# Kernel optimization log

Hardware: AMD Instinct MI355X
Metric: run time of the kernel (lower is better)

The kernel has to match this reference:

```python
import jax, jax.numpy as jnp
import numpy as np
import math

EPS = 1e-6
P_MIN = 1e-3
P_MAX = 10.0
NUM_ITERS = 3
REG = 1.0
K = 64       # num_clusters
D = 128      # cluster_dim
TOKEN = 256  # token_dim
B, N, C = 8, 8192, 512


def _l2norm(t):
    return t / jnp.clip(jnp.linalg.norm(t, axis=-1, keepdims=True), 1e-12)


def _mlp(h, W1, b1, W2, b2):
    # torch Linear: y = h @ W.T + b ; dropout is identity at eval
    return jax.nn.relu(h @ W1.T + b1) @ W2.T + b2


def _log_otp_solver(log_a, log_b, M, num_iters, reg):
    M = M / reg
    u = jnp.zeros_like(log_a)
    v = jnp.zeros_like(log_b)
    for _ in range(num_iters):  # fixed small iteration count
        u = log_a - jax.scipy.special.logsumexp(M + v[:, None, :], axis=2)
        v = log_b - jax.scipy.special.logsumexp(M + u[:, :, None], axis=1)
    return M + u[:, :, None] + v[:, None, :]


def _get_matching_probs(S, dustbin_score, num_iters, reg):
    b, m, n = S.shape
    dust_row = jnp.broadcast_to(dustbin_score, (b, 1, n)).astype(S.dtype)
    S_aug = jnp.concatenate([S, dust_row], axis=1)  # [b, m+1, n]
    norm = -math.log(n + m)
    log_a = jnp.full((m + 1,), norm, dtype=S.dtype).at[-1].add(math.log(n - m))
    log_a = jnp.broadcast_to(log_a, (b, m + 1))
    log_b = jnp.full((b, n), norm, dtype=S.dtype)
    log_P = _log_otp_solver(log_a, log_b, S_aug, num_iters, reg)
    return log_P - norm


def setup_inputs() -> dict:
    key = jax.random.key(0)
    ks = jax.random.split(key, 8)
    x = jax.random.normal(ks[0], (B, N, C), dtype=jnp.float32)

    def lin(k, fin, fout):
        k1, k2 = jax.random.split(k)
        W = 0.02 * jax.random.normal(k1, (fout, fin), dtype=jnp.float32)
        b = 0.02 * jax.random.normal(k2, (fout,), dtype=jnp.float32)
        return W, b

    tW1, tb1 = lin(ks[1], C, 512)
    tW2, tb2 = lin(ks[2], 512, TOKEN)
    cW1, cb1 = lin(ks[3], C, 512)
    cW2, cb2 = lin(ks[4], 512, D)
    sW1, sb1 = lin(ks[5], C, 512)
    sW2, sb2 = lin(ks[6], 512, K)
    # GeM p param init so that softplus(w)+p_min == 3.0
    gem_w = jnp.array([math.log(math.exp(3.0 - P_MIN) - 1.0)], dtype=jnp.float32)
    dust_bin = jnp.array(1.0, dtype=jnp.float32)
    return dict(x=x, gem_w=gem_w, dust_bin=dust_bin,
                tW1=tW1, tb1=tb1, tW2=tW2, tb2=tb2,
                cW1=cW1, cb1=cb1, cW2=cW2, cb2=cb2,
                sW1=sW1, sb1=sb1, sW2=sW2, sb2=sb2)


def reference(x, gem_w, dust_bin,
              tW1, tb1, tW2, tb2,
              cW1, cb1, cW2, cb2,
              sW1, sb1, sW2, sb2):
    # --- GeM pooling: [B, N, C] -> [B, C] ---
    p = jnp.minimum(jax.nn.softplus(gem_w) + P_MIN, P_MAX)  # [1]
    g = jnp.mean(jnp.clip(x.astype(jnp.float32), EPS, None) ** p, axis=1) ** (1.0 / p)
    g = jnp.where(jnp.isfinite(g), g, jnp.zeros_like(g))

    global_token = _mlp(g, tW1, tb1, tW2, tb2)          # [B, TOKEN]
    local = _mlp(x, cW1, cb1, cW2, cb2)                 # [B, N, D]
    scores = _mlp(x, sW1, sb1, sW2, sb2)                # [B, N, K]

    S = scores.transpose(0, 2, 1)                       # [B, K, N]
    log_P = _get_matching_probs(S, dust_bin, NUM_ITERS, REG)  # [B, K+1, N]
    p_mat = jnp.exp(log_P)[:, :-1, :]                   # drop dustbin -> [B, K, N]

    # aggregated[b, d, k] = sum_n local[b, n, d] * p[b, k, n]  (no O(B*D*K*N) blowup)
    agg = jnp.einsum('bnd,bkn->bdk', local, p_mat).reshape(x.shape[0], -1)  # [B, D*K]

    result = jnp.concatenate([_l2norm(global_token), _l2norm(agg)], axis=-1)
    return _l2norm(result)
```

## Files before the change

kernel.cpp:

```cpp
#include <hip/hip_runtime.h>
#include <hip/hip_bf16.h>
#include <math.h>

#define BB   8
#define NN   8192
#define CC   512
#define DD   128
#define KK   64
#define TOK  256
#define MM   (BB*NN)

typedef unsigned short u16;
typedef __attribute__((ext_vector_type(8))) short short8;
typedef __attribute__((ext_vector_type(4))) float floatx4;

struct PtrSz { const void* p[15]; int sz[15]; };

__device__ __forceinline__ float bf2f(u16 v) {
    union { unsigned u; float f; } x; x.u = ((unsigned)v) << 16; return x.f;
}
__device__ __forceinline__ u16 f2bf(float f) {
    union { float f; unsigned u; } x; x.f = f;
    unsigned r = x.u + 0x7fffu + ((x.u >> 16) & 1u);
    return (u16)(r >> 16);
}
__device__ __forceinline__ float nat_exp2(float a) {
    float r; asm("v_exp_f32 %0, %1" : "=v"(r) : "v"(a)); return r;
}
__device__ __forceinline__ float nat_log2(float a) {
    float r; asm("v_log_f32 %0, %1" : "=v"(r) : "v"(a)); return r;
}
__device__ __forceinline__ void gload16(const void* g, void* l) {
    __builtin_amdgcn_global_load_lds(
        (const __attribute__((address_space(1))) void*)g,
        (__attribute__((address_space(3))) void*)l, 16, 0, 0);
}

__global__ __launch_bounds__(256)
void fill_sentinel(float* __restrict__ out, int n, float val) {
    int i = blockIdx.x*256 + threadIdx.x;
    if (i < n) out[i] = val;
}

__global__ __launch_bounds__(256)
void detect_all(PtrSz ps, int* __restrict__ flags) {
    int i = blockIdx.x;
    const u16* q = (const u16*)ps.p[i];
    int m = ps.sz[i] < 4096 ? ps.sz[i] : 4096;
    __shared__ int cnt;
    if (threadIdx.x == 0) cnt = 0;
    __syncthreads();
    int c = 0;
    for (int j = threadIdx.x; j < m; j += 256) {
        int e = (q[j] >> 7) & 0xFF;
        if (e < 90 || e > 165) c++;
    }
    atomicAdd(&cnt, c);
    __syncthreads();
    if (threadIdx.x == 0) flags[i] = (cnt * 8 > m) ? 1 : 0;
}

#define W_TW1 0
#define W_TB1 262144
#define W_TW2 262656
#define W_TB2 393728
#define W_CW1 393984
#define W_CB1 656128
#define W_CW2 656640
#define W_CB2 722176
#define W_SW1 722304
#define W_SB1 984448
#define W_SW2 984960
#define W_SB2 1017728
#define W_TOTAL 1017792

__global__ __launch_bounds__(256)
void conv_weights(PtrSz ps, const int* __restrict__ flags,
                  u16* __restrict__ wbuf, float* __restrict__ wscal) {
    long gid = (long)blockIdx.x*256 + threadIdx.x;
    if (gid == 0) {
        float vb = bf2f(((const u16*)ps.p[1])[0]);
        float vf = ((const float*)ps.p[1])[0];
        wscal[0] = (fabsf(vb - 2.94694f) < 0.2f) ? vb : vf;
    } else if (gid == 1) {
        float vb = bf2f(((const u16*)ps.p[2])[0]);
        float vf = ((const float*)ps.p[2])[0];
        wscal[1] = (fabsf(vb - 1.0f) < 0.2f) ? vb : vf;
    }
    if (gid >= W_TOTAL) return;
    int idx; long off;
    if      (gid < W_TB1) { idx = 3;  off = W_TW1; }
    else if (gid < W_TW2) { idx = 4;  off = W_TB1; }
    else if (gid < W_TB2) { idx = 5;  off = W_TW2; }
    else if (gid < W_CW1) { idx = 6;  off = W_TB2; }
    else if (gid < W_CB1) { idx = 7;  off = W_CW1; }
    else if (gid < W_CW2) { idx = 8;  off = W_CB1; }
    else if (gid < W_CB2) { idx = 9;  off = W_CW2; }
    else if (gid < W_SW1) { idx = 10; off = W_CB2; }
    else if (gid < W_SB1) { idx = 11; off = W_SW1; }
    else if (gid < W_SW2) { idx = 12; off = W_SB1; }
    else if (gid < W_SB2) { idx = 13; off = W_SW2; }
    else                  { idx = 14; off = W_SB2; }
    long k = gid - off;
    bool f32in = flags[idx] != 0;
    wbuf[gid] = f32in ? f2bf(((const float*)ps.p[idx])[k]) : ((const u16*)ps.p[idx])[k];
}

__global__ __launch_bounds__(256)
void gem_partial(const void* __restrict__ x, const float* __restrict__ wscal,
                 const int* __restrict__ flags, float* __restrict__ gacc) {
    __shared__ float red[4][512];
    int b = blockIdx.x, ny = blockIdx.y;
    int tid  = threadIdx.x;
    int wave = tid >> 6, lane = tid & 63;
    bool f32in = (flags[0] != 0);
    float gw = wscal[0];
    float p  = fminf(log1pf(expf(gw)) + 1e-3f, 10.0f);
    int c0 = lane*8;
    float s[8];
#pragma unroll
    for (int j = 0; j < 8; ++j) s[j] = 0.f;
    size_t base = ((size_t)b*NN + (size_t)ny*64 + wave)*CC + c0;
    if (f32in) {
        const float* xf = (const float*)x;
#pragma unroll 4
        for (int n = 0; n < 64; n += 4) {
            const float* pf = xf + base + (size_t)n*CC;
            float4 x0 = *(const float4*)pf;
            float4 x1 = *(const float4*)(pf + 4);
            float xv[8] = {x0.x,x0.y,x0.z,x0.w,x1.x,x1.y,x1.z,x1.w};
#pragma unroll
            for (int j = 0; j < 8; ++j)
                s[j] += nat_exp2(p * nat_log2(fmaxf(xv[j], 1e-6f)));
        }
    } else {
        const u16* xu = (const u16*)x;
#pragma unroll 4
        for (int n = 0; n < 64; n += 4) {
            short8 v8 = *(const short8*)(xu + base + (size_t)n*CC);
#pragma unroll
            for (int j = 0; j < 8; ++j)
                s[j] += nat_exp2(p * nat_log2(fmaxf(bf2f((u16)v8[j]), 1e-6f)));
        }
    }
#pragma unroll
    for (int j = 0; j < 8; ++j) red[wave][c0 + j] = s[j];
    __syncthreads();
#pragma unroll
    for (int t = 0; t < 2; ++t) {
        int c = tid + t*256;
        float v = red[0][c] + red[1][c] + red[2][c] + red[3][c];
        atomicAdd(&gacc[b*CC + c], v);
    }
}

__global__ __launch_bounds__(256)
void gem_finalize(const float* __restrict__ gacc, const float* __restrict__ wscal,
                  float* __restrict__ g) {
    int i = blockIdx.x*256 + threadIdx.x;
    float gw = wscal[0];
    float p  = fminf(log1pf(expf(gw)) + 1e-3f, 10.0f);
    float m  = gacc[i] / (float)NN;
    float r  = powf(m, 1.0f/p);
    if (!isfinite(r)) r = 0.f;
    g[i] = r;
}

__global__ __launch_bounds__(512)
void token_mlp(const float* __restrict__ g, const u16* __restrict__ wbuf,
               float* __restrict__ t) {
    __shared__ float gs[CC];
    __shared__ float hs[512];
    int b = blockIdx.x, j = threadIdx.x;
    gs[j] = g[b*CC + j];
    __syncthreads();
    float a = bf2f(wbuf[W_TB1 + j]);
    const u16* w = wbuf + W_TW1 + (size_t)j*CC;
    for (int c = 0; c < CC; ++c) a += gs[c]*bf2f(w[c]);
    hs[j] = fmaxf(a, 0.f);
    __syncthreads();
    if (j < TOK) {
        float a2 = bf2f(wbuf[W_TB2 + j]);
        const u16* w2 = wbuf + W_TW2 + (size_t)j*512;
        for (int c = 0; c < 512; ++c) a2 += hs[c]*bf2f(w2[c]);
        t[b*TOK + j] = a2;
    }
}

template<int BN, int MODE, bool RELU, bool ARAW>
__global__ __launch_bounds__(256)
void gemm_bt(const void* __restrict__ A, const u16* __restrict__ W,
             const u16* __restrict__ bias, void* __restrict__ Cout,
             const int* __restrict__ flags, int N, int Ksz,
             size_t a_base, int bidx_ovr) {
    constexpr int WSUB_N = BN/32;
    extern __shared__ char smem[];
    u16* a_lds = (u16*)smem;
    u16* b_lds = (u16*)smem + 128*32;
    const int tid  = threadIdx.x;
    const int wave = tid >> 6, lane = tid & 63;
    const int wm = wave >> 1, wn = wave & 1;

    int bx = blockIdx.x, by = blockIdx.y;
    {
        int nbx = gridDim.x, nby = gridDim.y;
        int nwg = nbx*nby;
        if ((nwg & 7) == 0) {
            int lid = bx + by*nbx;
            int q = nwg >> 3;
            int t = (lid & 7)*q + (lid >> 3);
            by = t % nby;
            bx = t / nby;
        }
    }
    const int bm0 = bx * 128;
    const int bn0 = by * BN;
    const int fr = lane & 15;
    const int fk = (lane >> 4) * 8;
    const bool f32in = ARAW && (flags[0] != 0);

    floatx4 acc[4][WSUB_N];
#pragma unroll
    for (int i = 0; i < 4; ++i)
#pragma unroll
        for (int j = 0; j < WSUB_N; ++j) acc[i][j] = (floatx4){0.f,0.f,0.f,0.f};

    for (int k0 = 0; k0 < Ksz; k0 += 32) {
        if (f32in) {
#pragma unroll
            for (int part = 0; part < 2; ++part) {
                int chunk = part*256 + tid;
                int row = chunk >> 2, kc = (chunk & 3)*8;
                size_t gidx = a_base + (size_t)(bm0 + row)*Ksz + k0 + kc;
                const float* pf = (const float*)A + gidx;
                float4 x0 = *(const float4*)pf;
                float4 x1 = *(const float4*)(pf + 4);
                short8 vA;
                vA[0]=(short)f2bf(x0.x); vA[1]=(short)f2bf(x0.y);
                vA[2]=(short)f2bf(x0.z); vA[3]=(short)f2bf(x0.w);
                vA[4]=(short)f2bf(x1.x); vA[5]=(short)f2bf(x1.y);
                vA[6]=(short)f2bf(x1.z); vA[7]=(short)f2bf(x1.w);
                *(short8*)(a_lds + row*32 + kc) = vA;
            }
        } else {
#pragma unroll
            for (int part = 0; part < 2; ++part) {
                int cb = part*256 + wave*64;
                int mych = cb + lane;
                int row = mych >> 2, kc = (mych & 3)*8;
                gload16((const u16*)A + a_base + (size_t)(bm0 + row)*Ksz + k0 + kc,
                        a_lds + (size_t)cb*8);
            }
        }
#pragma unroll
        for (int part = 0; part < BN/64; ++part) {
            int cb = part*256 + wave*64;
            int mych = cb + lane;
            int row = mych >> 2, kc = (mych & 3)*8;
            gload16(W + (size_t)(bn0 + row)*Ksz + k0 + kc,
                    b_lds + (size_t)cb*8);
        }
        __syncthreads();
        short8 af[4], bfr[WSUB_N];
#pragma unroll
        for (int i = 0; i < 4; ++i)
            af[i] = *(const short8*)(a_lds + (wm*64 + i*16 + fr)*32 + fk);
#pragma unroll
        for (int j = 0; j < WSUB_N; ++j)
            bfr[j] = *(const short8*)(b_lds + (wn*WSUB_N*16 + j*16 + fr)*32 + fk);
#pragma unroll
        for (int i = 0; i < 4; ++i)
#pragma unroll
            for (int j = 0; j < WSUB_N; ++j)
                acc[i][j] = __builtin_amdgcn_mfma_f32_16x16x32_bf16(af[i], bfr[j], acc[i][j], 0, 0, 0);
        __syncthreads();
    }

    if constexpr (MODE == 0) {
        u16* C = (u16*)Cout;
#pragma unroll
        for (int i = 0; i < 4; ++i) {
            int row0 = wm*64 + i*16 + ((lane>>4)<<2);
#pragma unroll
            for (int j = 0; j < WSUB_N; ++j) {
                int col = wn*WSUB_N*16 + j*16 + fr;
                float bb = bf2f(bias[bn0+col]);
#pragma unroll
                for (int r = 0; r < 4; ++r) {
                    float v = acc[i][j][r] + bb;
                    if (RELU) v = fmaxf(v, 0.f);
                    C[(size_t)(bm0+row0+r)*N + (bn0+col)] = f2bf(v);
                }
            }
        }
    } else {
        const int bidx = (bidx_ovr >= 0) ? bidx_ovr : (bm0 >> 13);
        const int nin  = bm0 & 8191;
        if constexpr (MODE == 1) {
            u16* tr = (u16*)smem;
#pragma unroll
            for (int i = 0; i < 4; ++i) {
                int row0 = wm*64 + i*16 + ((lane>>4)<<2);
#pragma unroll
                for (int j = 0; j < WSUB_N; ++j) {
                    int col = wn*WSUB_N*16 + j*16 + fr;
                    float bb = bf2f(bias[bn0+col]);
#pragma unroll
                    for (int r = 0; r < 4; ++r) {
                        float v = acc[i][j][r] + bb;
                        if (RELU) v = fmaxf(v, 0.f);
                        tr[col*128 + row0 + r] = f2bf(v);
                    }
                }
            }
            __syncthreads();
            u16* O = (u16*)Cout;
#pragma unroll
            for (int c = 0; c < (BN*128)/256; ++c) {
                int flat = c*256 + tid;
                int dcol = flat >> 7, rr = flat & 127;
                O[(size_t)(bidx*BN + bn0 + dcol)*NN + nin + rr] = tr[dcol*128 + rr];
            }
        } else {
            float* tr = (float*)smem;
#pragma unroll
            for (int i = 0; i < 4; ++i) {
                int row0 = wm*64 + i*16 + ((lane>>4)<<2);
#pragma unroll
                for (int j = 0; j < WSUB_N; ++j) {
                    int col = wn*WSUB_N*16 + j*16 + fr;
                    float bb = bf2f(bias[bn0+col]);
#pragma unroll
                    for (int r = 0; r < 4; ++r) {
                        float v = acc[i][j][r] + bb;
                        if (RELU) v = fmaxf(v, 0.f);
                        tr[col*128 + row0 + r] = v;
                    }
                }
            }
            __syncthreads();
            float* O = (float*)Cout;
#pragma unroll
            for (int c = 0; c < (BN*128)/256; ++c) {
                int flat = c*256 + tid;
                int dcol = flat >> 7, rr = flat & 127;
                O[(size_t)(bidx*BN + bn0 + dcol)*NN + nin + rr] = tr[dcol*128 + rr];
            }
        }
    }
}

__global__ __launch_bounds__(256)
void sink_u(const float* __restrict__ ST, const float* __restrict__ v,
            const float* __restrict__ wscal, float* __restrict__ u) {
    int m = blockIdx.x, b = blockIdx.y, t = threadIdx.x;
    const float norm = -logf(8256.0f);
    float la = (m == 64) ? norm + logf(8128.0f) : norm;
    float dustf = wscal[1];
    const float* vb = v + (size_t)b*NN;
    float r[32];
    float mx = -1e30f;
    if (m < 64) {
        const float* row = ST + ((size_t)b*64 + m)*NN;
#pragma unroll
        for (int i = 0; i < 32; ++i) { int n = t + i*256; r[i] = row[n] + vb[n]; mx = fmaxf(mx, r[i]); }
    } else {
#pragma unroll
        for (int i = 0; i < 32; ++i) { int n = t + i*256; r[i] = dustf + vb[n]; mx = fmaxf(mx, r[i]); }
    }
#pragma unroll
    for (int off = 32; off; off >>= 1) mx = fmaxf(mx, __shfl_xor(mx, off));
    __shared__ float red[4];
    if ((t & 63) == 0) red[t>>6] = mx;
    __syncthreads();
    mx = fmaxf(fmaxf(red[0], red[1]), fmaxf(red[2], red[3]));
    __syncthreads();
    float s = 0.f;
#pragma unroll
    for (int i = 0; i < 32; ++i) s += expf(r[i] - mx);
#pragma unroll
    for (int off = 32; off; off >>= 1) s += __shfl_xor(s, off);
    if ((t & 63) == 0) red[t>>6] = s;
    __syncthreads();
    s = red[0] + red[1] + red[2] + red[3];
    if (t == 0) u[b*65 + m] = la - (mx + logf(s));
}

__global__ __launch_bounds__(256)
void sink_v(const float* __restrict__ ST, const float* __restrict__ u,
            const float* __restrict__ wscal, float* __restrict__ v) {
    int b = blockIdx.y;
    int n = blockIdx.x*256 + threadIdx.x;
    __shared__ float us[65];
    if (threadIdx.x < 65) us[threadIdx.x] = u[b*65 + threadIdx.x];
    __syncthreads();
    const float norm = -logf(8256.0f);
    float mx = wscal[1] + us[64];
    float s  = 1.0f;
    const float* col = ST + (size_t)b*64*NN + n;
    for (int m = 0; m < 64; ++m) {
        float tv = col[(size_t)m*NN] + us[m];
        float nm = fmaxf(mx, tv);
        s = s*expf(mx - nm) + expf(tv - nm);
        mx = nm;
    }
    v[(size_t)b*NN + n] = norm - (mx + logf(s));
}

__global__ __launch_bounds__(256)
void sink_p(const float* __restrict__ ST, const float* __restrict__ u,
            const float* __restrict__ v, u16* __restrict__ P) {
    int b = blockIdx.y;
    int n = blockIdx.x*256 + threadIdx.x;
    const float norm = -logf(8256.0f);
    float vn = v[(size_t)b*NN + n];
    for (int k = 0; k < 64; ++k) {
        float lp = ST[((size_t)b*64 + k)*NN + n] + u[b*65 + k] + vn - norm;
        P[((size_t)b*64 + k)*NN + n] = f2bf(expf(lp));
    }
}

__global__ __launch_bounds__(256)
void agg_mfma(const u16* __restrict__ localT, const u16* __restrict__ P,
              float* __restrict__ agg) {
    __shared__ u16 a_lds[128*32];
    __shared__ u16 b_lds[64*32];
    int b = blockIdx.y, ns = blockIdx.x;
    int n0 = ns*256;
    const int tid  = threadIdx.x;
    const int wave = tid >> 6, lane = tid & 63;
    const int wm = wave >> 1, wn = wave & 1;
    const int fr = lane & 15, fk = (lane >> 4)*8;

    floatx4 acc[4][2];
#pragma unroll
    for (int i = 0; i < 4; ++i)
#pragma unroll
        for (int j = 0; j < 2; ++j) acc[i][j] = (floatx4){0.f,0.f,0.f,0.f};

    for (int s = 0; s < 8; ++s) {
        int nk = n0 + s*32;
#pragma unroll
        for (int part = 0; part < 2; ++part) {
            int chunk = part*256 + tid;
            int row = chunk >> 2, kc = (chunk & 3)*8;
            short8 vA = *(const short8*)(localT + ((size_t)b*128 + row)*NN + nk + kc);
            *(short8*)(a_lds + row*32 + kc) = vA;
        }
        {
            int row = tid >> 2, kc = (tid & 3)*8;
            short8 vB = *(const short8*)(P + ((size_t)b*64 + row)*NN + nk + kc);
            *(short8*)(b_lds + row*32 + kc) = vB;
        }
        __syncthreads();
        short8 af[4], bfr[2];
#pragma unroll
        for (int i = 0; i < 4; ++i)
            af[i] = *(const short8*)(a_lds + (wm*64 + i*16 + fr)*32 + fk);
#pragma unroll
        for (int j = 0; j < 2; ++j)
            bfr[j] = *(const short8*)(b_lds + (wn*32 + j*16 + fr)*32 + fk);
#pragma unroll
        for (int i = 0; i < 4; ++i)
#pragma unroll
            for (int j = 0; j < 2; ++j)
                acc[i][j] = __builtin_amdgcn_mfma_f32_16x16x32_bf16(af[i], bfr[j], acc[i][j], 0, 0, 0);
        __syncthreads();
    }
#pragma unroll
    for (int i = 0; i < 4; ++i) {
        int d0 = wm*64 + i*16 + ((lane>>4)<<2);
#pragma unroll
        for (int j = 0; j < 2; ++j) {
            int k = wn*32 + j*16 + fr;
#pragma unroll
            for (int r = 0; r < 4; ++r)
                atomicAdd(&agg[(size_t)b*8192 + (d0+r)*64 + k], acc[i][j][r]);
        }
    }
}

__global__ __launch_bounds__(256)
void finalize_out(const float* __restrict__ tg, const float* __restrict__ agg,
                  float* __restrict__ out) {
    int b = blockIdx.x, tid = threadIdx.x;
    float tv = tg[b*TOK + tid];
    float s1 = tv*tv;
    const float* ab = agg + (size_t)b*8192;
    float av[32];
    float s2 = 0.f;
#pragma unroll
    for (int i = 0; i < 32; ++i) { av[i] = ab[tid + i*256]; s2 += av[i]*av[i]; }
#pragma unroll
    for (int off = 32; off; off >>= 1) { s1 += __shfl_xor(s1, off); s2 += __shfl_xor(s2, off); }
    __shared__ float r1[4], r2[4];
    int wave = tid >> 6, lane = tid & 63;
    if (lane == 0) { r1[wave] = s1; r2[wave] = s2; }
    __syncthreads();
    float S1 = r1[0]+r1[1]+r1[2]+r1[3];
    float S2 = r2[0]+r2[1]+r2[2]+r2[3];
    const float rs2 = 1.41421356237f;
    float sc1 = 1.0f/(fmaxf(sqrtf(S1), 1e-12f)*rs2);
    float sc2 = 1.0f/(fmaxf(sqrtf(S2), 1e-12f)*rs2);
    out[(size_t)b*8448 + tid] = tv*sc1;
#pragma unroll
    for (int i = 0; i < 32; ++i)
        out[(size_t)b*8448 + 256 + tid + i*256] = av[i]*sc2;
}

extern "C" void kernel_launch(void* const* d_in, const int* in_sizes, int n_in,
                              void* d_out, int out_size, void* d_ws, size_t ws_size,
                              hipStream_t stream) {
    float* out = (float*)d_out;

    static const int EXP[15] = {33554432,1,1,262144,512,131072,256,
                                262144,512,65536,128,262144,512,32768,64};
    bool ok = (n_in == 15) && (out_size == 67584);
    if (ok) for (int i = 0; i < 15; ++i) ok = ok && (in_sizes[i] == EXP[i]);
    if (!ok) {
        fill_sentinel<<<264, 256, 0, stream>>>(out, out_size, 0.25f);
        return;
    }
    const size_t NEED_BATCH = 52934656ull;
    if (ws_size < NEED_BATCH) {
        fill_sentinel<<<264, 256, 0, stream>>>(out, out_size, 0.5f);
        return;
    }

    const void* x = d_in[0];
    PtrSz ps;
    for (int i = 0; i < 15; ++i) { ps.p[i] = d_in[i]; ps.sz[i] = in_sizes[i]; }

    char* base = (char*)d_ws;
    float* gacc = (float*)(base + 0);
    float* u    = (float*)(base + 16384);
    float* v    = (float*)(base + 18464);
    float* agg  = (float*)(base + 280608);
    const size_t ZERO_BYTES = 542752;
    float* g    = (float*)(base + 542752);
    float* tglb = (float*)(base + 559136);
    int*   flags= (int*)  (base + 567328);
    float* wscal= (float*)(base + 567392);
    u16*   wbuf = (u16*)  (base + 567424);
    float* ST   = (float*)(base + 2603008);
    u16* localT = (u16*)  (base + 19380224);
    u16* P      = (u16*)  (base + 36157440);
    u16* h1     = (u16*)  (base + 44546048);
    const size_t FULL_NEED = 44546048ull + 67108864ull;
    const bool mono = (ws_size >= FULL_NEED);

    hipMemsetAsync(d_ws, 0, ZERO_BYTES, stream);

    detect_all<<<15, 256, 0, stream>>>(ps, flags);
    conv_weights<<<3977, 256, 0, stream>>>(ps, flags, wbuf, wscal);

    gem_partial<<<dim3(BB, 128), 256, 0, stream>>>(x, wscal, flags, gacc);
    gem_finalize<<<16, 256, 0, stream>>>(gacc, wscal, g);
    token_mlp<<<BB, 512, 0, stream>>>(g, wbuf, tglb);

    if (mono) {
        gemm_bt<128, 0, true,  true ><<<dim3(512, 4), 256, 16384, stream>>>(
            x, wbuf + W_CW1, wbuf + W_CB1, h1, flags, 512, 512, 0, -1);
        gemm_bt<128, 1, false, false><<<dim3(512, 1), 256, 32768, stream>>>(
            h1, wbuf + W_CW2, wbuf + W_CB2, localT, flags, 128, 512, 0, -1);
        gemm_bt<128, 0, true,  true ><<<dim3(512, 4), 256, 16384, stream>>>(
            x, wbuf + W_SW1, wbuf + W_SB1, h1, flags, 512, 512, 0, -1);
        gemm_bt< 64, 2, false, false><<<dim3(512, 1), 256, 32768, stream>>>(
            h1, wbuf + W_SW2, wbuf + W_SB2, ST, flags, 64, 512, 0, -1);
    } else {
        for (int b = 0; b < BB; ++b) {
            size_t ab = (size_t)b*NN*CC;
            gemm_bt<128, 0, true,  true ><<<dim3(64, 4), 256, 16384, stream>>>(
                x, wbuf + W_CW1, wbuf + W_CB1, h1, flags, 512, 512, ab, -1);
            gemm_bt<128, 1, false, false><<<dim3(64, 1), 256, 32768, stream>>>(
                h1, wbuf + W_CW2, wbuf + W_CB2, localT, flags, 128, 512, 0, b);
            gemm_bt<128, 0, true,  true ><<<dim3(64, 4), 256, 16384, stream>>>(
                x, wbuf + W_SW1, wbuf + W_SB1, h1, flags, 512, 512, ab, -1);
            gemm_bt< 64, 2, false, false><<<dim3(64, 1), 256, 32768, stream>>>(
                h1, wbuf + W_SW2, wbuf + W_SB2, ST, flags, 64, 512, 0, b);
        }
    }

    for (int it = 0; it < 3; ++it) {
        sink_u<<<dim3(65, BB), 256, 0, stream>>>(ST, v, wscal, u);
        sink_v<<<dim3(32, BB), 256, 0, stream>>>(ST, u, wscal, v);
    }
    sink_p<<<dim3(32, BB), 256, 0, stream>>>(ST, u, v, P);

    agg_mfma<<<dim3(32, BB), 256, 0, stream>>>(localT, P, agg);
    finalize_out<<<BB, 256, 0, stream>>>(tglb, agg, out);
}
```

Measured before the change: 513.3 us.

## Double-buffer GEMM LDS, fuse both first-layer MLPs, and fold P into the last Sinkhorn step

Gives the bf16-input GEMM path two LDS buffers so the load of the next K-slice overlaps MFMA work on the current one. The f32-input path stays single-buffered. When the workspace is large enough, both first-layer MLP GEMMs run in one launch over a 1024-wide h1, split by column block, and the second-layer GEMMs read their half through an lda stride. The MODE 0 epilogue is staged through LDS so it can write 16-byte vectors, and the final sink_v iteration writes P directly, which removes the separate sink_p pass. The cost is higher LDS usage per block, twice the h1 workspace, and 64 live registers in the fused sink kernel.

```diff
diff --git a/kernel.cpp b/kernel.cpp
--- a/kernel.cpp
+++ b/kernel.cpp
@@ -191,12 +191,18 @@
 __global__ __launch_bounds__(256)
 void gemm_bt(const void* __restrict__ A, const u16* __restrict__ W,
              const u16* __restrict__ bias, void* __restrict__ Cout,
-             const int* __restrict__ flags, int N, int Ksz,
-             size_t a_base, int bidx_ovr) {
+             const int* __restrict__ flags, int N, int Ksz, int lda,
+             size_t a_base, int bidx_ovr,
+             const u16* __restrict__ W_alt, const u16* __restrict__ bias_alt,
+             int nsplit) {
     constexpr int WSUB_N = BN/32;
+    constexpr int ATILE = 128*32;
+    constexpr int BTILE = BN*32;
     extern __shared__ char smem[];
-    u16* a_lds = (u16*)smem;
-    u16* b_lds = (u16*)smem + 128*32;
+    u16* a0 = (u16*)smem;
+    u16* b0 = a0 + ATILE;
+    u16* a1 = b0 + BTILE;
+    u16* b1 = a1 + ATILE;
     const int tid  = threadIdx.x;
     const int wave = tid >> 6, lane = tid & 63;
     const int wm = wave >> 1, wn = wave & 1;
@@ -213,8 +219,12 @@
             bx = t / nby;
         }
     }
+    const u16* Wp = W; const u16* bp = bias;
+    int byw = by;
+    if (W_alt != nullptr && by >= nsplit) { Wp = W_alt; bp = bias_alt; byw = by - nsplit; }
     const int bm0 = bx * 128;
     const int bn0 = by * BN;
+    const int bw0 = byw * BN;
     const int fr = lane & 15;
     const int fk = (lane >> 4) * 8;
     const bool f32in = ARAW && (flags[0] != 0);
@@ -225,13 +235,57 @@
 #pragma unroll
         for (int j = 0; j < WSUB_N; ++j) acc[i][j] = (floatx4){0.f,0.f,0.f,0.f};
 
-    for (int k0 = 0; k0 < Ksz; k0 += 32) {
-        if (f32in) {
+    auto STAGE = [&](u16* ab, u16* bb, int k0) {
+#pragma unroll
+        for (int part = 0; part < 2; ++part) {
+            int cb = part*256 + wave*64;
+            int mych = cb + lane;
+            int row = mych >> 2, kc = (mych & 3)*8;
+            gload16((const u16*)A + a_base + (size_t)(bm0 + row)*lda + k0 + kc,
+                    ab + (size_t)cb*8);
+        }
+#pragma unroll
+        for (int part = 0; part < BN/64; ++part) {
+            int cb = part*256 + wave*64;
+            int mych = cb + lane;
+            int row = mych >> 2, kc = (mych & 3)*8;
+            gload16(Wp + (size_t)(bw0 + row)*Ksz + k0 + kc,
+                    bb + (size_t)cb*8);
+        }
+    };
+    auto COMPUTE = [&](const u16* ab, const u16* bb) {
+        short8 af[4], bfr[WSUB_N];
+#pragma unroll
+        for (int i = 0; i < 4; ++i)
+            af[i] = *(const short8*)(ab + (wm*64 + i*16 + fr)*32 + fk);
+#pragma unroll
+        for (int j = 0; j < WSUB_N; ++j)
+            bfr[j] = *(const short8*)(bb + (wn*WSUB_N*16 + j*16 + fr)*32 + fk);
+#pragma unroll
+        for (int i = 0; i < 4; ++i)
+#pragma unroll
+            for (int j = 0; j < WSUB_N; ++j)
+                acc[i][j] = __builtin_amdgcn_mfma_f32_16x16x32_bf16(af[i], bfr[j], acc[i][j], 0, 0, 0);
+    };
+
+    if (!f32in) {
+        STAGE(a0, b0, 0);
+        __syncthreads();
+        for (int k0 = 0; k0 < Ksz; k0 += 64) {
+            if (k0 + 32 < Ksz) STAGE(a1, b1, k0 + 32);
+            COMPUTE(a0, b0);
+            __syncthreads();
+            if (k0 + 64 < Ksz) STAGE(a0, b0, k0 + 64);
+            COMPUTE(a1, b1);
+            __syncthreads();
+        }
+    } else {
+        for (int k0 = 0; k0 < Ksz; k0 += 32) {
 #pragma unroll
             for (int part = 0; part < 2; ++part) {
                 int chunk = part*256 + tid;
                 int row = chunk >> 2, kc = (chunk & 3)*8;
-                size_t gidx = a_base + (size_t)(bm0 + row)*Ksz + k0 + kc;
+                size_t gidx = a_base + (size_t)(bm0 + row)*lda + k0 + kc;
                 const float* pf = (const float*)A + gidx;
                 float4 x0 = *(const float4*)pf;
                 float4 x1 = *(const float4*)(pf + 4);
@@ -240,58 +294,47 @@
                 vA[2]=(short)f2bf(x0.z); vA[3]=(short)f2bf(x0.w);
                 vA[4]=(short)f2bf(x1.x); vA[5]=(short)f2bf(x1.y);
                 vA[6]=(short)f2bf(x1.z); vA[7]=(short)f2bf(x1.w);
-                *(short8*)(a_lds + row*32 + kc) = vA;
+                *(short8*)(a0 + row*32 + kc) = vA;
             }
-        } else {
-#pragma unroll
-            for (int part = 0; part < 2; ++part) {
+#pragma unroll
+            for (int part = 0; part < BN/64; ++part) {
                 int cb = part*256 + wave*64;
                 int mych = cb + lane;
                 int row = mych >> 2, kc = (mych & 3)*8;
-                gload16((const u16*)A + a_base + (size_t)(bm0 + row)*Ksz + k0 + kc,
-                        a_lds + (size_t)cb*8);
+                gload16(Wp + (size_t)(bw0 + row)*Ksz + k0 + kc,
+                        b0 + (size_t)cb*8);
             }
-        }
-#pragma unroll
-        for (int part = 0; part < BN/64; ++part) {
-            int cb = part*256 + wave*64;
-            int mych = cb + lane;
-            int row = mych >> 2, kc = (mych & 3)*8;
-            gload16(W + (size_t)(bn0 + row)*Ksz + k0 + kc,
-                    b_lds + (size_t)cb*8);
-        }
-        __syncthreads();
-        short8 af[4], bfr[WSUB_N];
-#pragma unroll
-        for (int i = 0; i < 4; ++i)
-            af[i] = *(const short8*)(a_lds + (wm*64 + i*16 + fr)*32 + fk);
-#pragma unroll
-        for (int j = 0; j < WSUB_N; ++j)
-            bfr[j] = *(const short8*)(b_lds + (wn*WSUB_N*16 + j*16 + fr)*32 + fk);
-#pragma unroll
-        for (int i = 0; i < 4; ++i)
-#pragma unroll
-            for (int j = 0; j < WSUB_N; ++j)
-                acc[i][j] = __builtin_amdgcn_mfma_f32_16x16x32_bf16(af[i], bfr[j], acc[i][j], 0, 0, 0);
-        __syncthreads();
+            __syncthreads();
+            COMPUTE(a0, b0);
+            __syncthreads();
+        }
     }
 
     if constexpr (MODE == 0) {
-        u16* C = (u16*)Cout;
+        u16* cs = (u16*)smem;
 #pragma unroll
         for (int i = 0; i < 4; ++i) {
             int row0 = wm*64 + i*16 + ((lane>>4)<<2);
 #pragma unroll
             for (int j = 0; j < WSUB_N; ++j) {
                 int col = wn*WSUB_N*16 + j*16 + fr;
-                float bb = bf2f(bias[bn0+col]);
+                float bb = bf2f(bp[bw0+col]);
 #pragma unroll
                 for (int r = 0; r < 4; ++r) {
                     float v = acc[i][j][r] + bb;
                     if (RELU) v = fmaxf(v, 0.f);
-                    C[(size_t)(bm0+row0+r)*N + (bn0+col)] = f2bf(v);
+                    cs[(row0+r)*BN + col] = f2bf(v);
                 }
             }
+        }
+        __syncthreads();
+        u16* C = (u16*)Cout;
+#pragma unroll
+        for (int c = 0; c < (128*BN)/(256*8); ++c) {
+            int flat = (c*256 + tid)*8;
+            int rowt = flat / BN, colt = flat % BN;
+            *(short8*)(C + (size_t)(bm0+rowt)*N + bn0 + colt) =
+                *(const short8*)(cs + flat);
         }
     } else {
         const int bidx = (bidx_ovr >= 0) ? bidx_ovr : (bm0 >> 13);
@@ -304,7 +347,7 @@
 #pragma unroll
                 for (int j = 0; j < WSUB_N; ++j) {
                     int col = wn*WSUB_N*16 + j*16 + fr;
-                    float bb = bf2f(bias[bn0+col]);
+                    float bb = bf2f(bp[bw0+col]);
 #pragma unroll
                     for (int r = 0; r < 4; ++r) {
                         float v = acc[i][j][r] + bb;
@@ -329,7 +372,7 @@
 #pragma unroll
                 for (int j = 0; j < WSUB_N; ++j) {
                     int col = wn*WSUB_N*16 + j*16 + fr;
-                    float bb = bf2f(bias[bn0+col]);
+                    float bb = bf2f(bp[bw0+col]);
 #pragma unroll
                     for (int r = 0; r < 4; ++r) {
                         float v = acc[i][j][r] + bb;
@@ -386,9 +429,11 @@
     if (t == 0) u[b*65 + m] = la - (mx + logf(s));
 }
 
-__global__ __launch_bounds__(256)
-void sink_v(const float* __restrict__ ST, const float* __restrict__ u,
-            const float* __restrict__ wscal, float* __restrict__ v) {
+template<int WP>
+__global__ __launch_bounds__(256)
+void sink_v_t(const float* __restrict__ ST, const float* __restrict__ u,
+              const float* __restrict__ wscal, float* __restrict__ v,
+              u16* __restrict__ P) {
     int b = blockIdx.y;
     int n = blockIdx.x*256 + threadIdx.x;
     __shared__ float us[65];
@@ -398,25 +443,28 @@
     float mx = wscal[1] + us[64];
     float s  = 1.0f;
     const float* col = ST + (size_t)b*64*NN + n;
-    for (int m = 0; m < 64; ++m) {
-        float tv = col[(size_t)m*NN] + us[m];
-        float nm = fmaxf(mx, tv);
-        s = s*expf(mx - nm) + expf(tv - nm);
-        mx = nm;
-    }
-    v[(size_t)b*NN + n] = norm - (mx + logf(s));
-}
-
-__global__ __launch_bounds__(256)
-void sink_p(const float* __restrict__ ST, const float* __restrict__ u,
-            const float* __restrict__ v, u16* __restrict__ P) {
-    int b = blockIdx.y;
-    int n = blockIdx.x*256 + threadIdx.x;
-    const float norm = -logf(8256.0f);
-    float vn = v[(size_t)b*NN + n];
-    for (int k = 0; k < 64; ++k) {
-        float lp = ST[((size_t)b*64 + k)*NN + n] + u[b*65 + k] + vn - norm;
-        P[((size_t)b*64 + k)*NN + n] = f2bf(expf(lp));
+    if (WP) {
+        float r[64];
+#pragma unroll
+        for (int m = 0; m < 64; ++m) {
+            r[m] = col[(size_t)m*NN] + us[m];
+            float nm = fmaxf(mx, r[m]);
+            s = s*expf(mx - nm) + expf(r[m] - nm);
+            mx = nm;
+        }
+        float vn = norm - (mx + logf(s));
+        v[(size_t)b*NN + n] = vn;
+#pragma unroll
+        for (int k = 0; k < 64; ++k)
+            P[((size_t)b*64 + k)*NN + n] = f2bf(expf(r[k] + vn - norm));
+    } else {
+        for (int m = 0; m < 64; ++m) {
+            float tv = col[(size_t)m*NN] + us[m];
+            float nm = fmaxf(mx, tv);
+            s = s*expf(mx - nm) + expf(tv - nm);
+            mx = nm;
+        }
+        v[(size_t)b*NN + n] = norm - (mx + logf(s));
     }
 }
 
@@ -546,8 +594,10 @@
     u16* localT = (u16*)  (base + 19380224);
     u16* P      = (u16*)  (base + 36157440);
     u16* h1     = (u16*)  (base + 44546048);
-    const size_t FULL_NEED = 44546048ull + 67108864ull;
-    const bool mono = (ws_size >= FULL_NEED);
+    const size_t FULL_NEED  = 44546048ull + 67108864ull;
+    const size_t FUSED_NEED = 44546048ull + 134217728ull;
+    const bool fused = (ws_size >= FUSED_NEED);
+    const bool mono  = (ws_size >= FULL_NEED);
 
     hipMemsetAsync(d_ws, 0, ZERO_BYTES, stream);
 
@@ -558,34 +608,55 @@
     gem_finalize<<<16, 256, 0, stream>>>(gacc, wscal, g);
     token_mlp<<<BB, 512, 0, stream>>>(g, wbuf, tglb);
 
-    if (mono) {
-        gemm_bt<128, 0, true,  true ><<<dim3(512, 4), 256, 16384, stream>>>(
-            x, wbuf + W_CW1, wbuf + W_CB1, h1, flags, 512, 512, 0, -1);
+    const int NOSPLIT = 1 << 30;
+    if (fused) {
+        gemm_bt<128, 0, true,  true ><<<dim3(512, 8), 256, 32768, stream>>>(
+            x, wbuf + W_CW1, wbuf + W_CB1, h1, flags, 1024, 512, 512, 0, -1,
+            wbuf + W_SW1, wbuf + W_SB1, 4);
         gemm_bt<128, 1, false, false><<<dim3(512, 1), 256, 32768, stream>>>(
-            h1, wbuf + W_CW2, wbuf + W_CB2, localT, flags, 128, 512, 0, -1);
-        gemm_bt<128, 0, true,  true ><<<dim3(512, 4), 256, 16384, stream>>>(
-            x, wbuf + W_SW1, wbuf + W_SB1, h1, flags, 512, 512, 0, -1);
+            h1, wbuf + W_CW2, wbuf + W_CB2, localT, flags, 128, 512, 1024, 0, -1,
+            nullptr, nullptr, NOSPLIT);
         gemm_bt< 64, 2, false, false><<<dim3(512, 1), 256, 32768, stream>>>(
-            h1, wbuf + W_SW2, wbuf + W_SB2, ST, flags, 64, 512, 0, -1);
+            h1, wbuf + W_SW2, wbuf + W_SB2, ST, flags, 64, 512, 1024, 512, -1,
+            nullptr, nullptr, NOSPLIT);
+    } else if (mono) {
+        gemm_bt<128, 0, true,  true ><<<dim3(512, 4), 256, 32768, stream>>>(
+            x, wbuf + W_CW1, wbuf + W_CB1, h1, flags, 512, 512, 512, 0, -1,
+            nullptr, nullptr, NOSPLIT);
+        gemm_bt<128, 1, false, false><<<dim3(512, 1), 256, 32768, stream>>>(
+            h1, wbuf + W_CW2, wbuf + W_CB2, localT, flags, 128, 512, 512, 0, -1,
+            nullptr, nullptr, NOSPLIT);
+        gemm_bt<128, 0, true,  true ><<<dim3(512, 4), 256, 32768, stream>>>(
+            x, wbuf + W_SW1, wbuf + W_SB1, h1, flags, 512, 512, 512, 0, -1,
+            nullptr, nullptr, NOSPLIT);
+        gemm_bt< 64, 2, false, false><<<dim3(512, 1), 256, 32768, stream>>>(
+            h1, wbuf + W_SW2, wbuf + W_SB2, ST, flags, 64, 512, 512, 0, -1,
+            nullptr, nullptr, NOSPLIT);
     } else {
         for (int b = 0; b < BB; ++b) {
             size_t ab = (size_t)b*NN*CC;
-            gemm_bt<128, 0, true,  true ><<<dim3(64, 4), 256, 16384, stream>>>(
-                x, wbuf + W_CW1, wbuf + W_CB1, h1, flags, 512, 512, ab, -1);
+            gemm_bt<128, 0, true,  true ><<<dim3(64, 4), 256, 32768, stream>>>(
+                x, wbuf + W_CW1, wbuf + W_CB1, h1, flags, 512, 512, 512, ab, -1,
+                nullptr, nullptr, NOSPLIT);
             gemm_bt<128, 1, false, false><<<dim3(64, 1), 256, 32768, stream>>>(
-                h1, wbuf + W_CW2, wbuf + W_CB2, localT, flags, 128, 512, 0, b);
-            gemm_bt<128, 0, true,  true ><<<dim3(64, 4), 256, 16384, stream>>>(
-                x, wbuf + W_SW1, wbuf + W_SB1, h1, flags, 512, 512, ab, -1);
+                h1, wbuf + W_CW2, wbuf + W_CB2, localT, flags, 128, 512, 512, 0, b,
+                nullptr, nullptr, NOSPLIT);
+            gemm_bt<128, 0, true,  true ><<<dim3(64, 4), 256, 32768, stream>>>(
+                x, wbuf + W_SW1, wbuf + W_SB1, h1, flags, 512, 512, 512, ab, -1,
+                nullptr, nullptr, NOSPLIT);
             gemm_bt< 64, 2, false, false><<<dim3(64, 1), 256, 32768, stream>>>(
-                h1, wbuf + W_SW2, wbuf + W_SB2, ST, flags, 64, 512, 0, b);
+                h1, wbuf + W_SW2, wbuf + W_SB2, ST, flags, 64, 512, 512, 0, b,
+                nullptr, nullptr, NOSPLIT);
         }
     }
 
     for (int it = 0; it < 3; ++it) {
         sink_u<<<dim3(65, BB), 256, 0, stream>>>(ST, v, wscal, u);
-        sink_v<<<dim3(32, BB), 256, 0, stream>>>(ST, u, wscal, v);
-    }
-    sink_p<<<dim3(32, BB), 256, 0, stream>>>(ST, u, v, P);
+        if (it == 2)
+            sink_v_t<1><<<dim3(32, BB), 256, 0, stream>>>(ST, u, wscal, v, P);
+        else
+            sink_v_t<0><<<dim3(32, BB), 256, 0, stream>>>(ST, u, wscal, v, P);
+    }
 
     agg_mfma<<<dim3(32, BB), 256, 0, stream>>>(localT, P, agg);
     finalize_out<<<BB, 256, 0, stream>>>(tglb, agg, out);
```

After: 547.1 us. +6.6%, slower.
